# Performance work log

Hardware: AMD Instinct MI355X
Metric: run time of the kernel (lower is better)

The kernel has to match this reference:

```python
import jax, jax.numpy as jnp
import numpy as np

NUM_BANDS = 30
SPLIT_FREQ = 30
M_PARAM = 1
DIM = 2048
BATCH = 16384


def _dct_mat(N):
    # Orthonormal DCT-II matrix D: dct(x) = x @ D.T, idct(y) = y @ D
    n = np.arange(N, dtype=np.float64)
    kk = n[:, None]
    M = np.cos(np.pi * (n + 0.5) * kk / N)
    s = np.full(N, np.sqrt(2.0 / N))
    s[0] = np.sqrt(1.0 / N)
    return jnp.asarray((M * s[:, None]).astype(np.float32))


def _band_scale(freq_weights, k, N):
    # Precompute the per-frequency scale vector the torch loop applies band-by-band.
    pts = np.linspace(0, N - 1, NUM_BANDS + 1).astype(np.int64)  # torch .long() truncation
    scale = jnp.ones((N,), dtype=freq_weights.dtype)
    for i in range(NUM_BANDS):
        s, e = int(pts[i]), int(pts[i + 1])
        if e <= SPLIT_FREQ:
            f = 1.0 + freq_weights[i] * k * (1.0 - i / NUM_BANDS)
        else:
            f = 1.0 - freq_weights[i] * k * (1.0 - (i - NUM_BANDS // M_PARAM) / NUM_BANDS)
        scale = scale.at[s:e].set(f)  # bands are disjoint; base is 1
    return scale


def setup_inputs() -> dict:
    key = jax.random.key(0)
    ks = jax.random.split(key, 6)
    g = 0.02  # small init like xavier_uniform with gain 0.5
    return {
        "x": jax.random.normal(ks[0], (BATCH, DIM), dtype=jnp.float32),
        "freq_weights": jnp.ones((NUM_BANDS,), dtype=jnp.float32),
        "k": jnp.float32(0.3),
        "W1": jax.random.normal(ks[1], (1024, DIM), dtype=jnp.float32) * g,
        "b1": jnp.zeros((1024,), dtype=jnp.float32),
        "W2": jax.random.normal(ks[2], (512, 1024), dtype=jnp.float32) * g,
        "b2": jnp.zeros((512,), dtype=jnp.float32),
        "Wmu": jax.random.normal(ks[3], (256, 512), dtype=jnp.float32) * g,
        "bmu": jnp.zeros((256,), dtype=jnp.float32),
        "Wlv": jax.random.normal(ks[4], (256, 512), dtype=jnp.float32) * g,
        "blv": jnp.zeros((256,), dtype=jnp.float32),
    }


def reference(x, freq_weights, k, W1, b1, W2, b2, Wmu, bmu, Wlv, blv):
    N = x.shape[-1]
    D = _dct_mat(N)
    # DCT -> per-band reweight -> IDCT, fused as two matmuls and one vector multiply
    xd = (x @ D.T) * _band_scale(freq_weights, k, N)
    xe = xd @ D
    h = jax.nn.relu(xe @ W1.T + b1)
    h = jax.nn.relu(h @ W2.T + b2)
    mu = h @ Wmu.T + bmu
    logvar = h @ Wlv.T + blv
    return (mu, logvar)
```

## Files before the change

kernel.cpp:

```cpp
#include <hip/hip_runtime.h>
#include <hip/hip_bf16.h>
#include <math.h>

#define DIM 2048
#define BATCH 16384

typedef __attribute__((ext_vector_type(8))) short short8;
typedef __attribute__((ext_vector_type(4))) short short4v;
typedef __attribute__((ext_vector_type(4))) float floatx4;
typedef unsigned short ushort_t;

__device__ __forceinline__ ushort_t f2bf(float f) {
    union { float f; unsigned u; } v; v.f = f;
    unsigned r = v.u + 0x7FFFu + ((v.u >> 16) & 1u);
    return (ushort_t)(r >> 16);
}

__global__ void k_scale(const float* __restrict__ fw, const float* __restrict__ kp,
                        float* __restrict__ s) {
    int n = blockIdx.x * blockDim.x + threadIdx.x;
    if (n >= DIM) return;
    float kv = kp[0];
    float f = 1.0f;
    for (int i = 0; i < 30; ++i) {
        long s0 = (long)((double)i       * (double)(DIM - 1) / 30.0);
        long e0 = (long)((double)(i + 1) * (double)(DIM - 1) / 30.0);
        if (n >= s0 && n < e0) {
            if (e0 <= 30)
                f = 1.0f + fw[i] * kv * (1.0f - (float)i / 30.0f);
            else
                f = 1.0f - fw[i] * kv * (1.0f - (float)(i - 30) / 30.0f);
        }
    }
    s[n] = f;
}

__global__ void k_gen_d(ushort_t* __restrict__ D, ushort_t* __restrict__ Dt) {
    int idx = blockIdx.x * blockDim.x + threadIdx.x;
    int r = idx >> 11;
    int c = idx & (DIM - 1);
    const float w  = 7.6699039394282058e-4f;
    const float s0 = 0.02209708691207961f;
    const float s1 = 0.03125f;
    int m1 = ((2 * c + 1) * r) & (4 * DIM - 1);
    int m2 = ((2 * r + 1) * c) & (4 * DIM - 1);
    float v1 = __cosf(w * (float)m1) * (r == 0 ? s0 : s1);
    float v2 = __cosf(w * (float)m2) * (c == 0 ? s0 : s1);
    D[idx]  = f2bf(v1);
    Dt[idx] = f2bf(v2);
}

#define U_W1   262144
#define U_W2    65536
#define U_WH    16384
__global__ void k_cast_w(const float* __restrict__ W1, const float* __restrict__ W2,
                         const float* __restrict__ Wmu, const float* __restrict__ Wlv,
                         ushort_t* __restrict__ W1bf, ushort_t* __restrict__ W2bf,
                         ushort_t* __restrict__ Wcat) {
    int i = blockIdx.x * blockDim.x + threadIdx.x;
    const float* src; ushort_t* dst; int u;
    if (i < U_W1)                    { src = W1;  dst = W1bf;             u = i; }
    else if (i < U_W1 + U_W2)        { src = W2;  dst = W2bf;             u = i - U_W1; }
    else if (i < U_W1 + U_W2 + U_WH) { src = Wmu; dst = Wcat;             u = i - U_W1 - U_W2; }
    else                             { src = Wlv; dst = Wcat + 8 * U_WH;  u = i - U_W1 - U_W2 - U_WH; }
    const float4* p = reinterpret_cast<const float4*>(src) + 2 * (size_t)u;
    float4 a = p[0], b = p[1];
    short8 r;
    r[0] = (short)f2bf(a.x); r[1] = (short)f2bf(a.y);
    r[2] = (short)f2bf(a.z); r[3] = (short)f2bf(a.w);
    r[4] = (short)f2bf(b.x); r[5] = (short)f2bf(b.y);
    r[6] = (short)f2bf(b.z); r[7] = (short)f2bf(b.w);
    *reinterpret_cast<short8*>(dst + 8 * (size_t)u) = r;
}

__global__ void k_cast_x(const float* __restrict__ in, ushort_t* __restrict__ out) {
    int i = blockIdx.x * blockDim.x + threadIdx.x;
    const float4* p = reinterpret_cast<const float4*>(in) + 2 * (size_t)i;
    float4 a = p[0], b = p[1];
    short8 r;
    r[0] = (short)f2bf(a.x); r[1] = (short)f2bf(a.y);
    r[2] = (short)f2bf(a.z); r[3] = (short)f2bf(a.w);
    r[4] = (short)f2bf(b.x); r[5] = (short)f2bf(b.y);
    r[6] = (short)f2bf(b.z); r[7] = (short)f2bf(b.w);
    *reinterpret_cast<short8*>(out + 8 * (size_t)i) = r;
}

__global__ void k_red(const float* __restrict__ P, ushort_t* __restrict__ out,
                      const float* __restrict__ scale, int n4, int n4row) {
    int i = blockIdx.x * blockDim.x + threadIdx.x;
    const float4* p = reinterpret_cast<const float4*>(P);
    float4 a = p[i], b = p[i + n4], c = p[i + 2 * n4], d = p[i + 3 * n4];
    float4 s;
    s.x = a.x + b.x + c.x + d.x;
    s.y = a.y + b.y + c.y + d.y;
    s.z = a.z + b.z + c.z + d.z;
    s.w = a.w + b.w + c.w + d.w;
    if (scale) {
        float4 sc = reinterpret_cast<const float4*>(scale)[i & (n4row - 1)];
        s.x *= sc.x; s.y *= sc.y; s.z *= sc.z; s.w *= sc.w;
    }
    short4v o;
    o[0] = (short)f2bf(s.x); o[1] = (short)f2bf(s.y);
    o[2] = (short)f2bf(s.z); o[3] = (short)f2bf(s.w);
    *reinterpret_cast<short4v*>(out + 4 * (size_t)i) = o;
}

template<int TM, int TN, int BK, int EPI, bool SK4>
__device__ __forceinline__ void gemm_core(
        const ushort_t* __restrict__ A, const ushort_t* __restrict__ B,
        ushort_t* __restrict__ Cb, float* __restrict__ Cf,
        const float* __restrict__ ep0, const float* __restrict__ ep1,
        int M, int N, int K, int KC) {
    constexpr int BM = 32 * TM;
    constexpr int BN = 32 * TN;
    constexpr int SEGS = BK / 8;
    constexpr int RSH  = (BK == 32) ? 1 : 0;
    constexpr int SSH  = (SEGS == 4) ? 2 : 3;
    __shared__ __align__(16) ushort_t As[BM * BK];
    __shared__ __align__(16) ushort_t Bs[BN * BK];

    const int tid  = threadIdx.x;
    const int lane = tid & 63;
    const int wave = tid >> 6;
    const int wm   = wave >> 1;
    const int wn   = wave & 1;
    const int q    = lane >> 4;
    const int l16  = lane & 15;

    const int tilesM = M / BM;
    const int tilesN = N / BN;
    int bid = (int)blockIdx.x;
    int sk = 0;
    if constexpr (SK4) { int nt = tilesM * tilesN; sk = bid / nt; bid = bid % nt; }
    const int xcd = bid & 7;
    const int j   = bid >> 3;
    const int bm  = xcd * (tilesM >> 3) + j / tilesN;
    const int bn  = j % tilesN;

    floatx4 acc[TM][TN];
    #pragma unroll
    for (int i = 0; i < TM; ++i)
        #pragma unroll
        for (int jj = 0; jj < TN; ++jj)
            acc[i][jj] = (floatx4){0.f, 0.f, 0.f, 0.f};

    const long aBase = (long)bm * BM * K + (long)sk * KC;
    const long bBase = (long)bn * BN * K + (long)sk * KC;
    const int  KLOOP = SK4 ? KC : K;

    for (int kt = 0; kt < KLOOP; kt += BK) {
        __syncthreads();
        #pragma unroll
        for (int i = 0; i < BM * BK / 2048; ++i) {
            int idx = tid + i * 256;
            int row = idx >> SSH, seg = idx & (SEGS - 1);
            int gseg = seg ^ ((row >> RSH) & (SEGS - 1));
            const ushort_t* g = A + aBase + (long)row * K + kt + gseg * 8;
            __builtin_amdgcn_global_load_lds(
                (const __attribute__((address_space(1))) void*)g,
                (__attribute__((address_space(3))) void*)(As + idx * 8),
                16, 0, 0);
        }
        #pragma unroll
        for (int i = 0; i < BN * BK / 2048; ++i) {
            int idx = tid + i * 256;
            int row = idx >> SSH, seg = idx & (SEGS - 1);
            int gseg = seg ^ ((row >> RSH) & (SEGS - 1));
            const ushort_t* g = B + bBase + (long)row * K + kt + gseg * 8;
            __builtin_amdgcn_global_load_lds(
                (const __attribute__((address_space(1))) void*)g,
                (__attribute__((address_space(3))) void*)(Bs + idx * 8),
                16, 0, 0);
        }
        __syncthreads();

        #pragma unroll
        for (int ks = 0; ks < BK / 32; ++ks) {
            short8 af[TM], bfr[TN];
            #pragma unroll
            for (int t = 0; t < TM; ++t) {
                int srow = wm * TM * 16 + t * 16 + l16;
                int rseg = (ks * 4 + q) ^ ((srow >> RSH) & (SEGS - 1));
                af[t] = *reinterpret_cast<const short8*>(&As[srow * BK + rseg * 8]);
            }
            #pragma unroll
            for (int t = 0; t < TN; ++t) {
                int srow = wn * TN * 16 + t * 16 + l16;
                int rseg = (ks * 4 + q) ^ ((srow >> RSH) & (SEGS - 1));
                bfr[t] = *reinterpret_cast<const short8*>(&Bs[srow * BK + rseg * 8]);
            }
            #pragma unroll
            for (int i = 0; i < TM; ++i)
                #pragma unroll
                for (int jj = 0; jj < TN; ++jj)
                    acc[i][jj] = __builtin_amdgcn_mfma_f32_16x16x32_bf16(
                        af[i], bfr[jj], acc[i][jj], 0, 0, 0);
        }
    }

    #pragma unroll
    for (int i = 0; i < TM; ++i) {
        #pragma unroll
        for (int jj = 0; jj < TN; ++jj) {
            #pragma unroll
            for (int r = 0; r < 4; ++r) {
                int row = bm * BM + wm * TM * 16 + i * 16 + q * 4 + r;
                int col = bn * BN + wn * TN * 16 + jj * 16 + l16;
                float v = acc[i][jj][r];
                if constexpr (EPI == 2) {
                    v += ep0[col];
                    v = v > 0.f ? v : 0.f;
                    Cb[(long)row * N + col] = f2bf(v);
                } else if constexpr (EPI == 3) {
                    const int half = N >> 1;
                    if (col < half)
                        Cf[(long)row * half + col] = v + ep0[col];
                    else
                        Cf[(long)M * half + (long)row * half + (col - half)] = v + ep1[col - half];
                } else {
                    Cf[(long)sk * M * N + (long)row * N + col] = v;
                }
            }
        }
    }
}

__global__ __launch_bounds__(512, 2) void g2_256(const ushort_t* __restrict__ A,
        const ushort_t* __restrict__ B, ushort_t* __restrict__ Cb,
        const float* __restrict__ bias, int M, int N, int K) {
    constexpr int BM = 256, BN = 256, BK = 64;
    __shared__ __align__(16) ushort_t As[2][BM * BK];
    __shared__ __align__(16) ushort_t Bs[2][BN * BK];

    const int tid  = threadIdx.x;
    const int lane = tid & 63;
    const int wave = tid >> 6;
    const int wm   = wave >> 2;
    const int wn   = wave & 3;
    const int q    = lane >> 4;
    const int l16  = lane & 15;

    const int tilesM = M / BM;
    const int tilesN = N / BN;
    int bid = (int)blockIdx.x;
    const int xcd = bid & 7;
    const int jb  = bid >> 3;
    const int bm  = xcd * (tilesM >> 3) + jb / tilesN;
    const int bn  = jb % tilesN;
    const int NT  = K / BK;

    const long aBase = (long)bm * BM * K;
    const long bBase = (long)bn * BN * K;

    floatx4 acc[8][4];
    #pragma unroll
    for (int i = 0; i < 8; ++i)
        #pragma unroll
        for (int j = 0; j < 4; ++j)
            acc[i][j] = (floatx4){0.f, 0.f, 0.f, 0.f};

#define STG_A(h, tt) do {                                                           \
        _Pragma("unroll")                                                           \
        for (int _g = 0; _g < 2; ++_g) {                                            \
            int _idx = _g * 512 + tid;                                              \
            int _r = _idx >> 3, _s = _idx & 7;                                      \
            int _gs = _s ^ (_r & 7);                                                \
            const ushort_t* _gp = A + aBase + (long)((h) * 128 + _r) * K            \
                                  + (tt) * BK + _gs * 8;                            \
            __builtin_amdgcn_global_load_lds(                                       \
                (const __attribute__((address_space(1))) void*)_gp,                 \
                (__attribute__((address_space(3))) void*)                           \
                    (&As[(tt) & 1][(h) * 8192 + _idx * 8]),                         \
                16, 0, 0);                                                          \
        } } while (0)
#define STG_B(h, tt) do {                                                           \
        _Pragma("unroll")                                                           \
        for (int _g = 0; _g < 2; ++_g) {                                            \
            int _idx = _g * 512 + tid;                                              \
            int _r = _idx >> 3, _s = _idx & 7;                                      \
            int _gs = _s ^ (_r & 7);                                                \
            const ushort_t* _gp = B + bBase + (long)((h) * 128 + _r) * K            \
                                  + (tt) * BK + _gs * 8;                            \
            __builtin_amdgcn_global_load_lds(                                       \
                (const __attribute__((address_space(1))) void*)_gp,                 \
                (__attribute__((address_space(3))) void*)                           \
                    (&Bs[(tt) & 1][(h) * 8192 + _idx * 8]),                         \
                16, 0, 0);                                                          \
        } } while (0)

#define RDA(dst, IB) do {                                                           \
        _Pragma("unroll")                                                           \
        for (int _i = 0; _i < 4; ++_i)                                              \
            _Pragma("unroll")                                                       \
            for (int _k = 0; _k < 2; ++_k) {                                        \
                int _sr = wm * 128 + ((IB) + _i) * 16 + l16;                        \
                int _rs = (_k * 4 + q) ^ (_sr & 7);                                 \
                dst[_i][_k] = *reinterpret_cast<const short8*>(                     \
                    &As[_buf][_sr * BK + _rs * 8]);                                 \
            } } while (0)
#define RDB(dst, JB) do {                                                           \
        _Pragma("unroll")                                                           \
        for (int _j = 0; _j < 2; ++_j)                                              \
            _Pragma("unroll")                                                       \
            for (int _k = 0; _k < 2; ++_k) {                                        \
                int _sr = wn * 64 + ((JB) + _j) * 16 + l16;                         \
                int _rs = (_k * 4 + q) ^ (_sr & 7);                                 \
                dst[_j][_k] = *reinterpret_cast<const short8*>(                     \
                    &Bs[_buf][_sr * BK + _rs * 8]);                                 \
            } } while (0)

#define MM(AF, BF, IB, JB) do {                                                     \
        __builtin_amdgcn_s_setprio(1);                                              \
        _Pragma("unroll")                                                           \
        for (int _k = 0; _k < 2; ++_k)                                              \
            _Pragma("unroll")                                                       \
            for (int _i = 0; _i < 4; ++_i)                                          \
                _Pragma("unroll")                                                   \
                for (int _j = 0; _j < 2; ++_j)                                      \
                    acc[(IB) + _i][(JB) + _j] =                                     \
                        __builtin_amdgcn_mfma_f32_16x16x32_bf16(                    \
                            AF[_i][_k], BF[_j][_k],                                 \
                            acc[(IB) + _i][(JB) + _j], 0, 0, 0);                    \
        __builtin_amdgcn_s_setprio(0);                                              \
    } while (0)

#define MID do { __builtin_amdgcn_s_barrier();                                      \
        asm volatile("s_waitcnt lgkmcnt(0)" ::: "memory");                          \
        __builtin_amdgcn_sched_barrier(0); } while (0)
#define ENDP do { __builtin_amdgcn_s_barrier();                                     \
        asm volatile("" ::: "memory"); } while (0)

    STG_A(0, 0); STG_A(1, 0); STG_B(0, 0); STG_B(1, 0);
    STG_A(0, 1); STG_A(1, 1); STG_B(0, 1); STG_B(1, 1);
    asm volatile("s_waitcnt vmcnt(8)" ::: "memory");
    __builtin_amdgcn_s_barrier();
    asm volatile("" ::: "memory");

    short8 alo[4][2], ahi[4][2], blo[2][2], bhi[2][2];

    for (int t = 0; t < NT; ++t) {
        const int _buf = t & 1;
        RDA(alo, 0);
        RDB(blo, 0);
        MID;
        MM(alo, blo, 0, 0);
        ENDP;
        RDB(bhi, 2);
        MID;
        MM(alo, bhi, 0, 2);
        ENDP;
        RDA(ahi, 4);
        if (t < NT - 2) { STG_B(0, t + 2); STG_B(1, t + 2); }
        MID;
        MM(ahi, blo, 4, 0);
        ENDP;
        if (t < NT - 2) { STG_A(0, t + 2); STG_A(1, t + 2); }
        __builtin_amdgcn_s_barrier();
        asm volatile("" ::: "memory");
        MM(ahi, bhi, 4, 2);
        if (t < NT - 2)
            asm volatile("s_waitcnt vmcnt(8)" ::: "memory");
        else if (t == NT - 2)
            asm volatile("s_waitcnt vmcnt(0)" ::: "memory");
        ENDP;
    }

#undef ENDP
#undef MID
#undef MM
#undef RDB
#undef RDA
#undef STG_B
#undef STG_A

    float bsv[4];
    #pragma unroll
    for (int j = 0; j < 4; ++j)
        bsv[j] = bias[bn * BN + wn * 64 + j * 16 + l16];
    #pragma unroll
    for (int i = 0; i < 8; ++i) {
        int row = bm * BM + wm * 128 + i * 16 + q * 4;
        #pragma unroll
        for (int j = 0; j < 4; ++j) {
            int col = bn * BN + wn * 64 + j * 16 + l16;
            #pragma unroll
            for (int r = 0; r < 4; ++r) {
                float v = acc[i][j][r] + bsv[j];
                v = v > 0.f ? v : 0.f;
                Cb[(long)(row + r) * N + col] = f2bf(v);
            }
        }
    }
}

template<int EPI>
__device__ __forceinline__ void gemm128_v2(
        const ushort_t* __restrict__ A, const ushort_t* __restrict__ B,
        ushort_t* __restrict__ Cb, float* __restrict__ Cf,
        const float* __restrict__ ep0, const float* __restrict__ ep1,
        int M, int N, int K) {
    constexpr int BM = 128, BN = 128, BK = 32;
    __shared__ __align__(16) ushort_t As[4][BM * BK];
    __shared__ __align__(16) ushort_t Bs[4][BN * BK];

    const int tid  = threadIdx.x;
    const int lane = tid & 63;
    const int wave = tid >> 6;
    const int wm   = wave >> 1;
    const int wn   = wave & 1;
    const int q    = lane >> 4;
    const int l16  = lane & 15;

    const int tilesM = M / BM;
    const int tilesN = N / BN;
    int bid = (int)blockIdx.x;
    const int xcd = bid & 7;
    const int jb  = bid >> 3;
    const int bm  = xcd * (tilesM >> 3) + jb / tilesN;
    const int bn  = jb % tilesN;
    const int NT  = K / BK;

    const long aBase = (long)bm * BM * K;
    const long bBase = (long)bn * BN * K;

    floatx4 acc[4][4];
    #pragma unroll
    for (int i = 0; i < 4; ++i)
        #pragma unroll
        for (int j = 0; j < 4; ++j)
            acc[i][j] = (floatx4){0.f, 0.f, 0.f, 0.f};

#define STAGE_A(t) do { int _sl = (t) & 3;                                          \
        _Pragma("unroll")                                                           \
        for (int _g = 0; _g < 2; ++_g) {                                            \
            int _idx = _g * 256 + tid;                                              \
            int _row = _idx >> 2, _seg = _idx & 3;                                  \
            int _gs = _seg ^ ((_row >> 1) & 3);                                     \
            const ushort_t* _gp = A + aBase + (long)_row * K + (t) * BK + _gs * 8;  \
            __builtin_amdgcn_global_load_lds(                                       \
                (const __attribute__((address_space(1))) void*)_gp,                 \
                (__attribute__((address_space(3))) void*)(&As[_sl][_idx * 8]),      \
                16, 0, 0);                                                          \
        } } while (0)
#define STAGE_B(t) do { int _sl = (t) & 3;                                          \
        _Pragma("unroll")                                                           \
        for (int _g = 0; _g < 2; ++_g) {                                            \
            int _idx = _g * 256 + tid;                                              \
            int _row = _idx >> 2, _seg = _idx & 3;                                  \
            int _gs = _seg ^ ((_row >> 1) & 3);                                     \
            const ushort_t* _gp = B + bBase + (long)_row * K + (t) * BK + _gs * 8;  \
            __builtin_amdgcn_global_load_lds(                                       \
                (const __attribute__((address_space(1))) void*)_gp,                 \
                (__attribute__((address_space(3))) void*)(&Bs[_sl][_idx * 8]),      \
                16, 0, 0);                                                          \
        } } while (0)

    STAGE_A(0); STAGE_B(0);
    STAGE_A(1); STAGE_B(1);
    STAGE_A(2); STAGE_B(2);
    asm volatile("s_waitcnt vmcnt(8)" ::: "memory");
    __builtin_amdgcn_s_barrier();
    asm volatile("" ::: "memory");

#define KTILE(tt, DOSTAGE, WAITOP) do {                                             \
        const int _slot = (tt) & 3;                                                 \
        short8 _bf[4], _af[4];                                                      \
        _Pragma("unroll")                                                           \
        for (int _j = 0; _j < 4; ++_j) {                                            \
            int _sr = wn * 64 + _j * 16 + l16;                                      \
            int _rs = q ^ ((_sr >> 1) & 3);                                         \
            _bf[_j] = *reinterpret_cast<const short8*>(&Bs[_slot][_sr * BK + _rs * 8]); \
        }                                                                           \
        _Pragma("unroll")                                                           \
        for (int _i = 0; _i < 4; ++_i) {                                            \
            int _sr = wm * 64 + _i * 16 + l16;                                      \
            int _rs = q ^ ((_sr >> 1) & 3);                                         \
            _af[_i] = *reinterpret_cast<const short8*>(&As[_slot][_sr * BK + _rs * 8]); \
        }                                                                           \
        if (DOSTAGE) { STAGE_A((tt) + 3); STAGE_B((tt) + 3); }                      \
        __builtin_amdgcn_s_setprio(1);                                              \
        _Pragma("unroll")                                                           \
        for (int _i = 0; _i < 4; ++_i)                                              \
            _Pragma("unroll")                                                       \
            for (int _j = 0; _j < 4; ++_j)                                          \
                acc[_i][_j] = __builtin_amdgcn_mfma_f32_16x16x32_bf16(              \
                    _af[_i], _bf[_j], acc[_i][_j], 0, 0, 0);                        \
        __builtin_amdgcn_s_setprio(0);                                              \
        asm volatile("s_waitcnt lgkmcnt(0)" ::: "memory");                          \
        __builtin_amdgcn_sched_barrier(0);                                          \
        WAITOP;                                                                     \
        __builtin_amdgcn_s_barrier();                                               \
        asm volatile("" ::: "memory");                                              \
    } while (0)

    int t = 0;
    for (; t < NT - 3; ++t) {
        KTILE(t, true, asm volatile("s_waitcnt vmcnt(8)" ::: "memory"));
    }
    KTILE(t, false, asm volatile("s_waitcnt vmcnt(4)" ::: "memory")); ++t;
    KTILE(t, false, asm volatile("s_waitcnt vmcnt(0)" ::: "memory")); ++t;
    KTILE(t, false, (void)0);

#undef KTILE
#undef STAGE_A
#undef STAGE_B

    #pragma unroll
    for (int i = 0; i < 4; ++i) {
        #pragma unroll
        for (int jj = 0; jj < 4; ++jj) {
            #pragma unroll
            for (int r = 0; r < 4; ++r) {
                int row = bm * BM + wm * 64 + i * 16 + q * 4 + r;
                int col = bn * BN + wn * 64 + jj * 16 + l16;
                float v = acc[i][jj][r];
                if constexpr (EPI == 2) {
                    v += ep0[col];
                    v = v > 0.f ? v : 0.f;
                    Cb[(long)row * N + col] = f2bf(v);
                } else {
                    const int half = N >> 1;
                    v += (col < half) ? ep0[col] : ep1[col - half];
                    if (col < half)
                        Cf[(long)row * half + col] = v;
                    else
                        Cf[(long)M * half + (long)row * half + (col - half)] = v;
                }
            }
        }
    }
}

__global__ __launch_bounds__(256) void g0p_sk(const ushort_t* A, const ushort_t* B,
        float* P, int M, int N, int K, int KC) {
    gemm_core<4, 4, 32, 4, true>(A, B, nullptr, P, nullptr, nullptr, M, N, K, KC);
}
__global__ __launch_bounds__(256) void g1p_sk(const ushort_t* A, const ushort_t* B,
        float* P, int M, int N, int K, int KC) {
    gemm_core<4, 4, 32, 4, true>(A, B, nullptr, P, nullptr, nullptr, M, N, K, KC);
}
__global__ __launch_bounds__(256, 2) void g3_h2(const ushort_t* A, const ushort_t* B,
        ushort_t* Cb, const float* ep0, int M, int N, int K) {
    gemm128_v2<2>(A, B, Cb, nullptr, ep0, nullptr, M, N, K);
}
__global__ __launch_bounds__(256, 2) void g4_head(const ushort_t* A, const ushort_t* B,
        float* Cf, const float* ep0, const float* ep1, int M, int N, int K) {
    gemm128_v2<3>(A, B, nullptr, Cf, ep0, ep1, M, N, K);
}

extern "C" void kernel_launch(void* const* d_in, const int* in_sizes, int n_in,
                              void* d_out, int out_size, void* d_ws, size_t ws_size,
                              hipStream_t stream) {
    const float* x   = (const float*)d_in[0];
    const float* fw  = (const float*)d_in[1];
    const float* kp  = (const float*)d_in[2];
    const float* W1  = (const float*)d_in[3];
    const float* b1  = (const float*)d_in[4];
    const float* W2  = (const float*)d_in[5];
    const float* b2  = (const float*)d_in[6];
    const float* Wmu = (const float*)d_in[7];
    const float* bmu = (const float*)d_in[8];
    const float* Wlv = (const float*)d_in[9];
    const float* blv = (const float*)d_in[10];
    float* out = (float*)d_out;

    char* ws = (char*)d_ws;
    const size_t MB = 1024 * 1024;
    ushort_t* W1bf = (ushort_t*)(ws + 0);
    ushort_t* Dbf  = (ushort_t*)(ws + 4   * MB);
    ushort_t* Dtbf = (ushort_t*)(ws + 12  * MB);
    ushort_t* T1sT = (ushort_t*)(ws + 20  * MB);
    ushort_t* H1   = (ushort_t*)(ws + 0);
    float*    P    = (float*)   (ws + 32  * MB);
    ushort_t* Xbf  = (ushort_t*)(ws + 32  * MB);
    ushort_t* H2   = (ushort_t*)(ws + 96  * MB);
    ushort_t* M1T  = (ushort_t*)(ws + 112 * MB);
    ushort_t* W2bf = (ushort_t*)(ws + 116 * MB);
    ushort_t* Wcat = (ushort_t*)(ws + 117 * MB);
    float*    svec = (float*)   (ws + 118 * MB);

    hipLaunchKernelGGL(k_scale, dim3(DIM / 256), dim3(256), 0, stream, fw, kp, svec);
    hipLaunchKernelGGL(k_gen_d, dim3(DIM * DIM / 256), dim3(256), 0, stream, Dbf, Dtbf);
    hipLaunchKernelGGL(k_cast_w, dim3((U_W1 + U_W2 + 2 * U_WH) / 256), dim3(256), 0, stream,
                       W1, W2, Wmu, Wlv, W1bf, W2bf, Wcat);

    hipLaunchKernelGGL(g0p_sk, dim3(8 * 16 * 4), dim3(256), 0, stream,
                       W1bf, Dbf, P, 1024, 2048, 2048, 512);
    hipLaunchKernelGGL(k_red, dim3(1024 * 2048 / 4 / 256), dim3(256), 0, stream,
                       P, T1sT, svec, 1024 * 2048 / 4, 2048 / 4);
    hipLaunchKernelGGL(g1p_sk, dim3(8 * 16 * 4), dim3(256), 0, stream,
                       T1sT, Dtbf, P, 1024, 2048, 2048, 512);
    hipLaunchKernelGGL(k_red, dim3(1024 * 2048 / 4 / 256), dim3(256), 0, stream,
                       P, M1T, nullptr, 1024 * 2048 / 4, 2048 / 4);

    hipLaunchKernelGGL(k_cast_x, dim3(BATCH * DIM / 8 / 256), dim3(256), 0, stream, x, Xbf);

    hipLaunchKernelGGL(g2_256, dim3((BATCH / 256) * (1024 / 256)), dim3(512), 0, stream,
                       Xbf, M1T, H1, b1, BATCH, 1024, 2048);
    hipLaunchKernelGGL(g3_h2, dim3((BATCH / 128) * (512 / 128)), dim3(256), 0, stream,
                       H1, W2bf, H2, b2, BATCH, 512, 1024);
    hipLaunchKernelGGL(g4_head, dim3((BATCH / 128) * (512 / 128)), dim3(256), 0, stream,
                       H2, Wcat, out, bmu, blv, BATCH, 512, 512);

    (void)in_sizes; (void)n_in; (void)out_size; (void)ws_size;
}
```

Baseline: 386.0 us.

## Software-pipeline LDS fragment reads ahead of MFMA phases in GEMM main loop

Restructures the GEMM main loop so that LDS fragment reads for the next phase, including the next tile's first fragments, are issued before the current MFMA block instead of waiting behind a barrier and lgkmcnt(0). The explicit per-phase lgkmcnt waits and sched barriers are removed, and a prologue plus two peeled epilogue iterations are added. The aim is to hide LDS latency under matrix-core work. In exchange, the wait on global-to-LDS loads becomes a full vmcnt(0) each iteration rather than a partial one, which may expose global load latency.

Measured after the change: 379.6 us. No clear change (-1.6%).

```diff
diff --git a/kernel.cpp b/kernel.cpp
--- a/kernel.cpp
+++ b/kernel.cpp
@@ -288,7 +288,7 @@
                 16, 0, 0);                                                          \
         } } while (0)
 
-#define RDA(dst, IB) do {                                                           \
+#define RDA(dst, IB, BUF) do {                                                      \
         _Pragma("unroll")                                                           \
         for (int _i = 0; _i < 4; ++_i)                                              \
             _Pragma("unroll")                                                       \
@@ -296,9 +296,9 @@
                 int _sr = wm * 128 + ((IB) + _i) * 16 + l16;                        \
                 int _rs = (_k * 4 + q) ^ (_sr & 7);                                 \
                 dst[_i][_k] = *reinterpret_cast<const short8*>(                     \
-                    &As[_buf][_sr * BK + _rs * 8]);                                 \
+                    &As[(BUF)][_sr * BK + _rs * 8]);                                \
             } } while (0)
-#define RDB(dst, JB) do {                                                           \
+#define RDB(dst, JB, BUF) do {                                                      \
         _Pragma("unroll")                                                           \
         for (int _j = 0; _j < 2; ++_j)                                              \
             _Pragma("unroll")                                                       \
@@ -306,7 +306,7 @@
                 int _sr = wn * 64 + ((JB) + _j) * 16 + l16;                         \
                 int _rs = (_k * 4 + q) ^ (_sr & 7);                                 \
                 dst[_j][_k] = *reinterpret_cast<const short8*>(                     \
-                    &Bs[_buf][_sr * BK + _rs * 8]);                                 \
+                    &Bs[(BUF)][_sr * BK + _rs * 8]);                                \
             } } while (0)
 
 #define MM(AF, BF, IB, JB) do {                                                     \
@@ -324,49 +324,65 @@
         __builtin_amdgcn_s_setprio(0);                                              \
     } while (0)
 
-#define MID do { __builtin_amdgcn_s_barrier();                                      \
-        asm volatile("s_waitcnt lgkmcnt(0)" ::: "memory");                          \
-        __builtin_amdgcn_sched_barrier(0); } while (0)
-#define ENDP do { __builtin_amdgcn_s_barrier();                                     \
+#define BAR do { asm volatile("" ::: "memory");                                     \
+        __builtin_amdgcn_s_barrier();                                               \
         asm volatile("" ::: "memory"); } while (0)
+
+    short8 alo[4][2], ahi[4][2], blo[2][2], bhi[2][2];
 
     STG_A(0, 0); STG_A(1, 0); STG_B(0, 0); STG_B(1, 0);
     STG_A(0, 1); STG_A(1, 1); STG_B(0, 1); STG_B(1, 1);
     asm volatile("s_waitcnt vmcnt(8)" ::: "memory");
-    __builtin_amdgcn_s_barrier();
-    asm volatile("" ::: "memory");
-
-    short8 alo[4][2], ahi[4][2], blo[2][2], bhi[2][2];
-
-    for (int t = 0; t < NT; ++t) {
-        const int _buf = t & 1;
-        RDA(alo, 0);
-        RDB(blo, 0);
-        MID;
+    BAR;
+    RDA(alo, 0, 0);
+    RDB(blo, 0, 0);
+
+    int t = 0;
+    for (; t < NT - 2; ++t) {
+        const int buf = t & 1, nbuf = buf ^ 1;
+        RDB(bhi, 2, buf);
         MM(alo, blo, 0, 0);
-        ENDP;
-        RDB(bhi, 2);
-        MID;
+        BAR;
+        RDA(ahi, 4, buf);
         MM(alo, bhi, 0, 2);
-        ENDP;
-        RDA(ahi, 4);
-        if (t < NT - 2) { STG_B(0, t + 2); STG_B(1, t + 2); }
-        MID;
+        asm volatile("s_waitcnt vmcnt(0)" ::: "memory");
+        BAR;
+        RDA(alo, 0, nbuf);
+        STG_B(0, t + 2); STG_B(1, t + 2);
         MM(ahi, blo, 4, 0);
-        ENDP;
-        if (t < NT - 2) { STG_A(0, t + 2); STG_A(1, t + 2); }
-        __builtin_amdgcn_s_barrier();
-        asm volatile("" ::: "memory");
+        BAR;
+        RDB(blo, 0, nbuf);
+        STG_A(0, t + 2); STG_A(1, t + 2);
         MM(ahi, bhi, 4, 2);
-        if (t < NT - 2)
-            asm volatile("s_waitcnt vmcnt(8)" ::: "memory");
-        else if (t == NT - 2)
-            asm volatile("s_waitcnt vmcnt(0)" ::: "memory");
-        ENDP;
-    }
-
-#undef ENDP
-#undef MID
+        BAR;
+    }
+    {
+        const int buf = t & 1, nbuf = buf ^ 1;
+        RDB(bhi, 2, buf);
+        MM(alo, blo, 0, 0);
+        BAR;
+        RDA(ahi, 4, buf);
+        MM(alo, bhi, 0, 2);
+        asm volatile("s_waitcnt vmcnt(0)" ::: "memory");
+        BAR;
+        RDA(alo, 0, nbuf);
+        MM(ahi, blo, 4, 0);
+        BAR;
+        RDB(blo, 0, nbuf);
+        MM(ahi, bhi, 4, 2);
+        BAR;
+    }
+    {
+        const int buf = (NT - 1) & 1;
+        RDB(bhi, 2, buf);
+        MM(alo, blo, 0, 0);
+        RDA(ahi, 4, buf);
+        MM(alo, bhi, 0, 2);
+        MM(ahi, blo, 4, 0);
+        MM(ahi, bhi, 4, 2);
+    }
+
+#undef BAR
 #undef MM
 #undef RDB
 #undef RDA
```
